# Performance work log

Measured on AMD Instinct MI355X. Metric: run time of the kernel, lower is better.

The kernel has to match this reference:

```python
import jax, jax.numpy as jnp
import numpy as np

# ---- geometry / physics constants (from setup_params) ----
H = 400; W_CROP = 400
PSF_W = 121          # interpolated_psf_width
CLEAR = 20           # clear_dist
_m = int(np.ceil(PSF_W / 2 - CLEAR + 2))
MARGIN = _m + _m % 2                    # 44
IM = H + 2 * MARGIN                     # 488
MAG = 100.0; PX_CCD = 11.0              # M, pixel_size_CCD
NZ = 64; Z_MIN = -2.0; Z_MAX = 2.0      # psf bank z sampling
SIGMA_READ = 10.0                       # read noise std (counts)
N_EMIT = 2048


def setup_inputs() -> dict:
    key = jax.random.key(0)
    k1, k2, k3, k4 = jax.random.split(key, 4)
    # emitter positions (um): xy in [-15,15] (stays inside canvas), z in [-2,2]
    lo = jnp.array([-15.0, -15.0, Z_MIN], jnp.float32)
    hi = jnp.array([15.0, 15.0, Z_MAX], jnp.float32)
    local_xyz = jax.random.uniform(k1, (1, N_EMIT, 3), jnp.float32) * (hi - lo) + lo
    Nphotons = jax.random.uniform(k2, (1, N_EMIT), jnp.float32) * 4000.0 + 1000.0
    xy_center = jnp.zeros((2,), jnp.float32)  # FOV center; unused when fd_flag=False
    psf_bank = jax.random.uniform(k3, (NZ, PSF_W, PSF_W), jnp.float32)  # positive PSFs
    noise_map = jax.random.normal(k4, (H, W_CROP), jnp.float32)         # unit gaussians
    return {"local_xyz": local_xyz, "Nphotons": Nphotons, "xy_center": xy_center,
            "psf_bank": psf_bank, "noise_map": noise_map}


def reference(local_xyz, Nphotons, xy_center, psf_bank, noise_map):
    x = local_xyz[0, :, 0]                       # [N] um
    y = local_xyz[0, :, 1]
    z = local_xyz[0, :, 2]
    nph = Nphotons[0]                            # [N]

    # psf_module(0,0,z): nearest-z lookup in precomputed bank (fd_flag=False)
    zi = jnp.clip(jnp.round((z - Z_MIN) / (Z_MAX - Z_MIN) * (NZ - 1)),
                  0, NZ - 1).astype(jnp.int32)
    psf = psf_bank[zi]                           # [N, PSF_W, PSF_W]

    # emitter position in camera pixels
    lx = x * MAG / PX_CCD
    ly = y * MAG / PX_CCD
    r0f = ly + IM / 2 - PSF_W / 2
    c0f = lx + IM / 2 - PSF_W / 2
    r0 = jnp.floor(r0f).astype(jnp.int32)        # [N] integer splat origin
    c0 = jnp.floor(c0f).astype(jnp.int32)
    rs = (r0f - jnp.floor(r0f))[:, None, None]   # sub-pixel shift in [0,1)
    cs = (c0f - jnp.floor(c0f))[:, None, None]

    # sub-pixel shift (bilinear, zero-fill boundary): out[i,j] = in[i-rs, j-cs]
    P = jnp.pad(psf, ((0, 0), (1, 0), (1, 0)))
    sh = ((1 - rs) * (1 - cs) * P[:, 1:, 1:] + rs * (1 - cs) * P[:, :-1, 1:]
          + (1 - rs) * cs * P[:, 1:, :-1] + rs * cs * P[:, :-1, :-1])
    sh = jnp.abs(sh)
    sh = sh / sh.sum(axis=(1, 2), keepdims=True) * nph[:, None, None]

    # scatter-add splat into shared canvas
    ar = jnp.arange(PSF_W, dtype=jnp.int32)
    rows = r0[:, None, None] + ar[None, :, None]  # [N, PSF_W, 1]
    cols = c0[:, None, None] + ar[None, None, :]  # [N, 1, PSF_W]
    canvas = jnp.zeros((IM, IM), sh.dtype).at[rows, cols].add(sh)

    im = canvas[MARGIN:MARGIN + H, MARGIN:MARGIN + W_CROP]

    # NoiseLayer: Gaussian approx of Poisson shot + read noise
    im_noisy = im + jnp.sqrt(jnp.maximum(im, 0.0) + SIGMA_READ ** 2) * noise_map

    # project_01 normalization
    return (im_noisy - im_noisy.min()) / (im_noisy.max() - im_noisy.min())
```

## Files before the change

### kernel.cpp

```cpp
#include <hip/hip_runtime.h>

#define H        400
#define W_CROP   400
#define PSF_W    121
#define MARGIN   44
#define IM       488
#define NZ       64
#define N_EMIT   2048
#define PSF_AREA (PSF_W * PSF_W)
#define SIGMA2   100.0f
#define TILE     16
#define TB       25
#define NTILES   (TB * TB)
#define NPIX     (H * W_CROP)
#define PADW     152
#define PADA     (PADW * PADW)
#define CHUNKS   4
#define CAPC     224
#define CAP_B    512
#define NBUCK    (TB * CHUNKS)
#define PADBLK   512

static __device__ __forceinline__ unsigned enc_ord(float f) {
    unsigned u = __float_as_uint(f);
    return (u & 0x80000000u) ? ~u : (u | 0x80000000u);
}
static __device__ __forceinline__ float dec_ord(unsigned u) {
    return __uint_as_float((u & 0x80000000u) ? (u & 0x7fffffffu) : ~u);
}

static __device__ __forceinline__ void geom_of(const float* __restrict__ xyz, int e,
                                               int& r0, int& c0, int& zi,
                                               float& r0f, float& c0f) {
    const float x = xyz[3 * e + 0];
    const float y = xyz[3 * e + 1];
    const float z = xyz[3 * e + 2];
    const float lx = (x * 100.0f) / 11.0f;
    const float ly = (y * 100.0f) / 11.0f;
    r0f = (ly + 244.0f) - 60.5f;
    c0f = (lx + 244.0f) - 60.5f;
    r0 = (int)floorf(r0f);
    c0 = (int)floorf(c0f);
    zi = (int)rintf((z + 2.0f) / 4.0f * 63.0f);
    zi = min(max(zi, 0), NZ - 1);
}

__global__ __launch_bounds__(256) void prep_kernel(
        const float* __restrict__ psf_bank, float* __restrict__ zpart,
        float* __restrict__ pad, unsigned* __restrict__ minmax,
        const float* __restrict__ xyz, const float* __restrict__ nph_arr,
        float4* __restrict__ bucket, int* __restrict__ bcnt)
{
    __shared__ float red[4][4];
    __shared__ int   wtot[4];

    if (blockIdx.x < PADBLK) {
        const int zi   = blockIdx.x >> 3;
        const int part = blockIdx.x & 7;

        if (blockIdx.x == 0 && threadIdx.x == 0) { minmax[0] = 0xFFFFFFFFu; minmax[1] = 0u; }

        const float* __restrict__ src = psf_bank + (size_t)zi * PSF_AREA;
        float* __restrict__ dst = pad + (size_t)zi * PADA;

        const int plo = part * 2888;
        const int phi = min(plo + 2888, PADA);
        for (int i = plo + (int)threadIdx.x; i < phi; i += 256) {
            const int rp = i / PADW;
            const int r = rp - 16;
            const int c = i - rp * PADW - 16;
            const bool in = ((unsigned)r < (unsigned)PSF_W) && ((unsigned)c < (unsigned)PSF_W);
            dst[i] = in ? src[r * PSF_W + c] : 0.0f;
        }

        const int slo = part * 1831;
        const int shi = min(slo + 1831, PSF_AREA);
        float S = 0.f, R = 0.f, C = 0.f, K = 0.f;
        for (int i = slo + (int)threadIdx.x; i < shi; i += 256) {
            const float v = src[i];
            const int r = i / PSF_W;
            const int c = i - r * PSF_W;
            S += v;
            if (r == PSF_W - 1) R += v;
            if (c == PSF_W - 1) C += v;
            if (r == PSF_W - 1 && c == PSF_W - 1) K += v;
        }
        #pragma unroll
        for (int off = 32; off > 0; off >>= 1) {
            S += __shfl_down(S, off, 64);
            R += __shfl_down(R, off, 64);
            C += __shfl_down(C, off, 64);
            K += __shfl_down(K, off, 64);
        }
        const int wave = threadIdx.x >> 6, lane = threadIdx.x & 63;
        if (lane == 0) { red[wave][0] = S; red[wave][1] = R; red[wave][2] = C; red[wave][3] = K; }
        __syncthreads();
        if (threadIdx.x == 0) {
            float4 o;
            o.x = (red[0][0] + red[1][0]) + (red[2][0] + red[3][0]);
            o.y = (red[0][1] + red[1][1]) + (red[2][1] + red[3][1]);
            o.z = (red[0][2] + red[1][2]) + (red[2][2] + red[3][2]);
            o.w = (red[0][3] + red[1][3]) + (red[2][3] + red[3][3]);
            *(float4*)(zpart + (size_t)(zi * 8 + part) * 4) = o;
        }
        return;
    }

    const int b   = blockIdx.x - PADBLK;
    const int btr = b >> 2, bzc = b & 3;
    const int w    = threadIdx.x >> 6;
    const int lane = threadIdx.x & 63;

    int mycnt = 0;
    unsigned mymask = 0u;
    #pragma unroll
    for (int q = 0; q < 8; ++q) {
        const int e = (int)threadIdx.x * 8 + q;
        int r0, c0, zi; float r0f, c0f;
        geom_of(xyz, e, r0, c0, zi, r0f, c0f);
        const bool p = ((zi >> 4) == bzc)
                     && (btr >= ((r0 - MARGIN) >> 4)) && (btr <= ((r0 + 76) >> 4));
        mymask |= (unsigned)p << q;
        mycnt += (int)p;
    }

    int incl = mycnt;
    #pragma unroll
    for (int off = 1; off < 64; off <<= 1) {
        const int v = __shfl_up(incl, off, 64);
        if (lane >= off) incl += v;
    }
    if (lane == 63) wtot[w] = incl;
    __syncthreads();
    int base = incl - mycnt;
    #pragma unroll
    for (int ww = 0; ww < 4; ++ww) base += (ww < w) ? wtot[ww] : 0;
    const int ntot = wtot[0] + wtot[1] + wtot[2] + wtot[3];

    if (mymask) {
        int slot = base;
        #pragma unroll
        for (int q = 0; q < 8; ++q) {
            if (mymask & (1u << q)) {
                const int e = (int)threadIdx.x * 8 + q;
                int r0, c0, zi; float r0f, c0f;
                geom_of(xyz, e, r0, c0, zi, r0f, c0f);
                if (slot < CAP_B) {
                    const float rs = r0f - floorf(r0f);
                    const float cs = c0f - floorf(c0f);
                    const float nph = nph_arr[e];
                    float4 s0, s1;
                    s0.x = nph * (1.0f - rs) * (1.0f - cs);
                    s0.y = nph * (1.0f - rs) * cs;
                    s0.z = nph * rs * (1.0f - cs);
                    s0.w = nph * rs * cs;
                    const int packed = ((r0 + 16) << 15) | ((c0 + 16) << 6) | zi;
                    s1.x = rs; s1.y = cs; s1.z = __int_as_float(packed); s1.w = 0.f;
                    bucket[(size_t)(b * CAP_B + slot) * 2]     = s0;
                    bucket[(size_t)(b * CAP_B + slot) * 2 + 1] = s1;
                }
                ++slot;
            }
        }
    }
    if (threadIdx.x == 0) bcnt[b] = min(ntot, CAP_B);
}

__global__ __launch_bounds__(256) void gather_kernel(
        const float* __restrict__ pad, const float4* __restrict__ bucket,
        const int* __restrict__ bcnt, const float* __restrict__ zpart,
        float* __restrict__ parts)
{
    const int zc   = (blockIdx.x & 7) >> 1;
    const int tile = 2 * (blockIdx.x >> 3) + (blockIdx.x & 1);
    if (tile >= NTILES) return;

    __shared__ float4 smeta[2 * CAPC];
    __shared__ float  tilepart[4][256];
    __shared__ int    wtot[4];

    const int tr = tile / TB, tc = tile - tr * TB;
    const int w    = threadIdx.x >> 6;
    const int lane = threadIdx.x & 63;
    const int px = lane & 15;
    const int wy = lane >> 4;
    const int orow0 = tr * TILE + wy * 4;
    const int ocol  = tc * TILE + px;
    const int crow0 = orow0 + MARGIN;
    const int ccol  = ocol + MARGIN;
    const int tcb   = (crow0 * PADW + ccol) * 4;
    const char* __restrict__ pbase = (const char*)pad;

    const int b   = tr * CHUNKS + zc;
    const int n_b = bcnt[b];
    const float4* __restrict__ bk = bucket + (size_t)b * CAP_B * 2;

    int nstaged = 0;
    for (int base_i = 0; base_i < n_b; base_i += 256) {
        const int i = base_i + (int)threadIdx.x;
        float4 m0, m1;
        int r0 = 0, c0 = 0, zi = 0;
        bool p = false;
        if (i < n_b) {
            m0 = bk[2 * i];
            m1 = bk[2 * i + 1];
            const int packed = __float_as_int(m1.z);
            zi = packed & 63;
            c0 = ((packed >> 6) & 511) - 16;
            r0 = ((packed >> 15) & 511) - 16;
            p = (tc >= ((c0 - MARGIN) >> 4)) && (tc <= ((c0 + 76) >> 4));
        }
        int incl = (int)p;
        #pragma unroll
        for (int off = 1; off < 64; off <<= 1) {
            const int v = __shfl_up(incl, off, 64);
            if (lane >= off) incl += v;
        }
        if (lane == 63) wtot[w] = incl;
        __syncthreads();
        int slot = nstaged + incl - (int)p;
        #pragma unroll
        for (int ww = 0; ww < 4; ++ww) slot += (ww < w) ? wtot[ww] : 0;
        const int round_tot = wtot[0] + wtot[1] + wtot[2] + wtot[3];
        if (p && slot < CAPC) {
            const float rs = m1.x, cs = m1.y;
            const float4* __restrict__ zp = (const float4*)zpart + zi * 8;
            float4 zm = zp[0];
            #pragma unroll
            for (int u = 1; u < 8; ++u) {
                const float4 t = zp[u];
                zm.x += t.x; zm.y += t.y; zm.z += t.z; zm.w += t.w;
            }
            const float ssum = zm.x - rs * zm.y - cs * zm.z + rs * cs * zm.w;
            const float inv = 1.0f / ssum;
            float4 s0, s1;
            s0.x = m0.x * inv; s0.y = m0.y * inv; s0.z = m0.z * inv; s0.w = m0.w * inv;
            const int offb = (zi * PADA + (15 - r0) * PADW + (16 - c0)) * 4;
            s1.x = __int_as_float(offb);
            s1.y = __int_as_float(r0);
            s1.z = __int_as_float(c0);
            s1.w = 0.f;
            smeta[2 * slot]     = s0;
            smeta[2 * slot + 1] = s1;
        }
        nstaged += round_tot;
        __syncthreads();
    }
    const int n = min(nstaged, CAPC);

    float acc0[4] = {0.f, 0.f, 0.f, 0.f};
    float acc1[4] = {0.f, 0.f, 0.f, 0.f};
    float acc2[4] = {0.f, 0.f, 0.f, 0.f};
    float acc3[4] = {0.f, 0.f, 0.f, 0.f};

    auto body = [&](int j, float* acc) {
        const float4 wt = smeta[2 * j];
        const float4 mm = smeta[2 * j + 1];
        const int off = __float_as_int(mm.x);
        const int pr0 = crow0 - __float_as_int(mm.y);
        const int pc  = ccol  - __float_as_int(mm.z);
        const char* __restrict__ p = pbase + (tcb + off);
        float a[5], b2[5];
        #pragma unroll
        for (int i = 0; i < 5; ++i) a[i] = *(const float*)(p + i * (PADW * 4));
        #pragma unroll
        for (int i = 0; i < 5; ++i) b2[i] = __shfl_up(a[i], 1, 16);
        if (px == 0) {
            #pragma unroll
            for (int i = 0; i < 5; ++i) b2[i] = *(const float*)(p - 4 + i * (PADW * 4));
        }
        const bool pcok = (unsigned)pc <= 120u;
        #pragma unroll
        for (int k = 0; k < 4; ++k) {
            float v = wt.x * a[k + 1];
            v = fmaf(wt.y, b2[k + 1], v);
            v = fmaf(wt.z, a[k],      v);
            v = fmaf(wt.w, b2[k],     v);
            const bool ok = pcok & ((unsigned)(pr0 + k) <= 120u);
            acc[k] += ok ? v : 0.f;
        }
    };

    int j = w;
    for (; j + 12 < n; j += 16) {
        body(j, acc0); body(j + 4, acc1); body(j + 8, acc2); body(j + 12, acc3);
    }
    for (; j < n; j += 4) body(j, acc0);

    #pragma unroll
    for (int k = 0; k < 4; ++k)
        tilepart[w][(wy * 4 + k) * 16 + px] = (acc0[k] + acc1[k]) + (acc2[k] + acc3[k]);
    __syncthreads();

    const int row = threadIdx.x >> 4, col = threadIdx.x & 15;
    const float s = ((tilepart[0][threadIdx.x] + tilepart[1][threadIdx.x]) +
                     (tilepart[2][threadIdx.x] + tilepart[3][threadIdx.x]));
    parts[(size_t)zc * NPIX + (tr * TILE + row) * W_CROP + (tc * TILE + col)] = s;
}

__global__ __launch_bounds__(256) void noise_minmax_kernel(
        const float* __restrict__ parts, const float* __restrict__ noise,
        float* __restrict__ out, unsigned* __restrict__ minmax)
{
    const int i = blockIdx.x * 256 + threadIdx.x;
    float vmin = 1e30f, vmax = -1e30f;
    if (i < NPIX / 4) {
        const float4 p0 = ((const float4*)parts)[i];
        const float4 p1 = ((const float4*)(parts + NPIX))[i];
        const float4 p2 = ((const float4*)(parts + 2 * NPIX))[i];
        const float4 p3 = ((const float4*)(parts + 3 * NPIX))[i];
        float4 im;
        im.x = (p0.x + p1.x) + (p2.x + p3.x);
        im.y = (p0.y + p1.y) + (p2.y + p3.y);
        im.z = (p0.z + p1.z) + (p2.z + p3.z);
        im.w = (p0.w + p1.w) + (p2.w + p3.w);
        const float4 nz = ((const float4*)noise)[i];
        im.x += sqrtf(fmaxf(im.x, 0.f) + SIGMA2) * nz.x;
        im.y += sqrtf(fmaxf(im.y, 0.f) + SIGMA2) * nz.y;
        im.z += sqrtf(fmaxf(im.z, 0.f) + SIGMA2) * nz.z;
        im.w += sqrtf(fmaxf(im.w, 0.f) + SIGMA2) * nz.w;
        ((float4*)out)[i] = im;
        vmin = fminf(fminf(im.x, im.y), fminf(im.z, im.w));
        vmax = fmaxf(fmaxf(im.x, im.y), fmaxf(im.z, im.w));
    }
    #pragma unroll
    for (int off = 32; off > 0; off >>= 1) {
        vmin = fminf(vmin, __shfl_down(vmin, off, 64));
        vmax = fmaxf(vmax, __shfl_down(vmax, off, 64));
    }
    if ((threadIdx.x & 63) == 0) {
        atomicMin(&minmax[0], enc_ord(vmin));
        atomicMax(&minmax[1], enc_ord(vmax));
    }
}

__global__ __launch_bounds__(256) void finalize_kernel(float* __restrict__ out,
                                                       const unsigned* __restrict__ minmax)
{
    const int i = blockIdx.x * 256 + threadIdx.x;
    if (i >= NPIX / 4) return;
    const float mn = dec_ord(minmax[0]);
    const float inv = 1.0f / (dec_ord(minmax[1]) - mn);
    float4 v = ((float4*)out)[i];
    v.x = (v.x - mn) * inv;
    v.y = (v.y - mn) * inv;
    v.z = (v.z - mn) * inv;
    v.w = (v.w - mn) * inv;
    ((float4*)out)[i] = v;
}

extern "C" void kernel_launch(void* const* d_in, const int* in_sizes, int n_in,
                              void* d_out, int out_size, void* d_ws, size_t ws_size,
                              hipStream_t stream) {
    const float* xyz      = (const float*)d_in[0];
    const float* nph      = (const float*)d_in[1];
    const float* psf_bank = (const float*)d_in[3];
    const float* noise    = (const float*)d_in[4];
    float* out = (float*)d_out;

    char* ws = (char*)d_ws;
    unsigned* minmax = (unsigned*)(ws + 0);
    float*    zpart  = (float*)(ws + 1024);
    float*    pad    = (float*)(ws + 9216);
    float4*   bucket = (float4*)(ws + 5923840);
    int*      bcnt   = (int*)(ws + 7562240);
    float*    parts  = (float*)(ws + 7563264);

    prep_kernel<<<PADBLK + NBUCK, 256, 0, stream>>>(psf_bank, zpart, pad, minmax,
                                                    xyz, nph, bucket, bcnt);
    gather_kernel<<<2504, 256, 0, stream>>>(pad, bucket, bcnt, zpart, parts);
    noise_minmax_kernel<<<(NPIX / 4 + 255) / 256, 256, 0, stream>>>(parts, noise, out, minmax);
    finalize_kernel<<<(NPIX / 4 + 255) / 256, 256, 0, stream>>>(out, minmax);
}
```

Baseline: 65.03 us.

## Split prep into pad and bucket kernels, precompute normalized weights in bucket stage

```diff
diff --git a/kernel.cpp b/kernel.cpp
--- a/kernel.cpp
+++ b/kernel.cpp
@@ -19,7 +19,6 @@
 #define CAPC     224
 #define CAP_B    512
 #define NBUCK    (TB * CHUNKS)
-#define PADBLK   512
 
 static __device__ __forceinline__ unsigned enc_ord(float f) {
     unsigned u = __float_as_uint(f);
@@ -45,68 +44,61 @@
     zi = min(max(zi, 0), NZ - 1);
 }
 
-__global__ __launch_bounds__(256) void prep_kernel(
+__global__ __launch_bounds__(256) void pad_zsum_kernel(
         const float* __restrict__ psf_bank, float* __restrict__ zpart,
-        float* __restrict__ pad, unsigned* __restrict__ minmax,
+        float* __restrict__ pad, unsigned* __restrict__ minmax)
+{
+    __shared__ float red[4][4];
+    const int zi   = blockIdx.x >> 3;
+    const int part = blockIdx.x & 7;
+
+    if (blockIdx.x == 0 && threadIdx.x == 0) { minmax[0] = 0xFFFFFFFFu; minmax[1] = 0u; }
+
+    const float* __restrict__ src = psf_bank + (size_t)zi * PSF_AREA;
+    float* __restrict__ dst = pad + (size_t)zi * PADA;
+
+    const int plo = part * 2888;
+    const int phi = min(plo + 2888, PADA);
+    float S = 0.f, R = 0.f, C = 0.f, K = 0.f;
+    for (int i = plo + (int)threadIdx.x; i < phi; i += 256) {
+        const int rp = i / PADW;
+        const int r = rp - 16;
+        const int c = i - rp * PADW - 16;
+        const bool in = ((unsigned)r < (unsigned)PSF_W) && ((unsigned)c < (unsigned)PSF_W);
+        const float v = in ? src[r * PSF_W + c] : 0.0f;
+        dst[i] = v;
+        S += v;
+        if (r == PSF_W - 1) R += v;
+        if (c == PSF_W - 1) C += v;
+        if (r == PSF_W - 1 && c == PSF_W - 1) K += v;
+    }
+    #pragma unroll
+    for (int off = 32; off > 0; off >>= 1) {
+        S += __shfl_down(S, off, 64);
+        R += __shfl_down(R, off, 64);
+        C += __shfl_down(C, off, 64);
+        K += __shfl_down(K, off, 64);
+    }
+    const int wave = threadIdx.x >> 6, lane = threadIdx.x & 63;
+    if (lane == 0) { red[wave][0] = S; red[wave][1] = R; red[wave][2] = C; red[wave][3] = K; }
+    __syncthreads();
+    if (threadIdx.x == 0) {
+        float4 o;
+        o.x = (red[0][0] + red[1][0]) + (red[2][0] + red[3][0]);
+        o.y = (red[0][1] + red[1][1]) + (red[2][1] + red[3][1]);
+        o.z = (red[0][2] + red[1][2]) + (red[2][2] + red[3][2]);
+        o.w = (red[0][3] + red[1][3]) + (red[2][3] + red[3][3]);
+        *(float4*)(zpart + (size_t)(zi * 8 + part) * 4) = o;
+    }
+}
+
+__global__ __launch_bounds__(256) void bucket_kernel(
         const float* __restrict__ xyz, const float* __restrict__ nph_arr,
+        const float* __restrict__ zpart,
         float4* __restrict__ bucket, int* __restrict__ bcnt)
 {
-    __shared__ float red[4][4];
-    __shared__ int   wtot[4];
-
-    if (blockIdx.x < PADBLK) {
-        const int zi   = blockIdx.x >> 3;
-        const int part = blockIdx.x & 7;
-
-        if (blockIdx.x == 0 && threadIdx.x == 0) { minmax[0] = 0xFFFFFFFFu; minmax[1] = 0u; }
-
-        const float* __restrict__ src = psf_bank + (size_t)zi * PSF_AREA;
-        float* __restrict__ dst = pad + (size_t)zi * PADA;
-
-        const int plo = part * 2888;
-        const int phi = min(plo + 2888, PADA);
-        for (int i = plo + (int)threadIdx.x; i < phi; i += 256) {
-            const int rp = i / PADW;
-            const int r = rp - 16;
-            const int c = i - rp * PADW - 16;
-            const bool in = ((unsigned)r < (unsigned)PSF_W) && ((unsigned)c < (unsigned)PSF_W);
-            dst[i] = in ? src[r * PSF_W + c] : 0.0f;
-        }
-
-        const int slo = part * 1831;
-        const int shi = min(slo + 1831, PSF_AREA);
-        float S = 0.f, R = 0.f, C = 0.f, K = 0.f;
-        for (int i = slo + (int)threadIdx.x; i < shi; i += 256) {
-            const float v = src[i];
-            const int r = i / PSF_W;
-            const int c = i - r * PSF_W;
-            S += v;
-            if (r == PSF_W - 1) R += v;
-            if (c == PSF_W - 1) C += v;
-            if (r == PSF_W - 1 && c == PSF_W - 1) K += v;
-        }
-        #pragma unroll
-        for (int off = 32; off > 0; off >>= 1) {
-            S += __shfl_down(S, off, 64);
-            R += __shfl_down(R, off, 64);
-            C += __shfl_down(C, off, 64);
-            K += __shfl_down(K, off, 64);
-        }
-        const int wave = threadIdx.x >> 6, lane = threadIdx.x & 63;
-        if (lane == 0) { red[wave][0] = S; red[wave][1] = R; red[wave][2] = C; red[wave][3] = K; }
-        __syncthreads();
-        if (threadIdx.x == 0) {
-            float4 o;
-            o.x = (red[0][0] + red[1][0]) + (red[2][0] + red[3][0]);
-            o.y = (red[0][1] + red[1][1]) + (red[2][1] + red[3][1]);
-            o.z = (red[0][2] + red[1][2]) + (red[2][2] + red[3][2]);
-            o.w = (red[0][3] + red[1][3]) + (red[2][3] + red[3][3]);
-            *(float4*)(zpart + (size_t)(zi * 8 + part) * 4) = o;
-        }
-        return;
-    }
-
-    const int b   = blockIdx.x - PADBLK;
+    __shared__ int wtot[4];
+    const int b   = blockIdx.x;
     const int btr = b >> 2, bzc = b & 3;
     const int w    = threadIdx.x >> 6;
     const int lane = threadIdx.x & 63;
@@ -148,14 +140,25 @@
                 if (slot < CAP_B) {
                     const float rs = r0f - floorf(r0f);
                     const float cs = c0f - floorf(c0f);
-                    const float nph = nph_arr[e];
+                    const float4* __restrict__ zp = (const float4*)zpart + zi * 8;
+                    float4 zm = zp[0];
+                    #pragma unroll
+                    for (int u = 1; u < 8; ++u) {
+                        const float4 t = zp[u];
+                        zm.x += t.x; zm.y += t.y; zm.z += t.z; zm.w += t.w;
+                    }
+                    const float ssum = zm.x - rs * zm.y - cs * zm.z + rs * cs * zm.w;
+                    const float s = nph_arr[e] / ssum;
                     float4 s0, s1;
-                    s0.x = nph * (1.0f - rs) * (1.0f - cs);
-                    s0.y = nph * (1.0f - rs) * cs;
-                    s0.z = nph * rs * (1.0f - cs);
-                    s0.w = nph * rs * cs;
-                    const int packed = ((r0 + 16) << 15) | ((c0 + 16) << 6) | zi;
-                    s1.x = rs; s1.y = cs; s1.z = __int_as_float(packed); s1.w = 0.f;
+                    s0.x = s * (1.0f - rs) * (1.0f - cs);
+                    s0.y = s * (1.0f - rs) * cs;
+                    s0.z = s * rs * (1.0f - cs);
+                    s0.w = s * rs * cs;
+                    const int offb = (zi * PADA + (15 - r0) * PADW + (16 - c0)) * 4;
+                    s1.x = __int_as_float(offb);
+                    s1.y = __int_as_float(r0);
+                    s1.z = __int_as_float(c0);
+                    s1.w = 0.f;
                     bucket[(size_t)(b * CAP_B + slot) * 2]     = s0;
                     bucket[(size_t)(b * CAP_B + slot) * 2 + 1] = s1;
                 }
@@ -168,8 +171,7 @@
 
 __global__ __launch_bounds__(256) void gather_kernel(
         const float* __restrict__ pad, const float4* __restrict__ bucket,
-        const int* __restrict__ bcnt, const float* __restrict__ zpart,
-        float* __restrict__ parts)
+        const int* __restrict__ bcnt, float* __restrict__ parts)
 {
     const int zc   = (blockIdx.x & 7) >> 1;
     const int tile = 2 * (blockIdx.x >> 3) + (blockIdx.x & 1);
@@ -199,49 +201,24 @@
     for (int base_i = 0; base_i < n_b; base_i += 256) {
         const int i = base_i + (int)threadIdx.x;
         float4 m0, m1;
-        int r0 = 0, c0 = 0, zi = 0;
         bool p = false;
         if (i < n_b) {
             m0 = bk[2 * i];
             m1 = bk[2 * i + 1];
-            const int packed = __float_as_int(m1.z);
-            zi = packed & 63;
-            c0 = ((packed >> 6) & 511) - 16;
-            r0 = ((packed >> 15) & 511) - 16;
+            const int c0 = __float_as_int(m1.z);
             p = (tc >= ((c0 - MARGIN) >> 4)) && (tc <= ((c0 + 76) >> 4));
         }
-        int incl = (int)p;
-        #pragma unroll
-        for (int off = 1; off < 64; off <<= 1) {
-            const int v = __shfl_up(incl, off, 64);
-            if (lane >= off) incl += v;
-        }
-        if (lane == 63) wtot[w] = incl;
+        const unsigned long long m = __ballot(p);
+        const int before = __popcll(m & ((1ULL << lane) - 1ULL));
+        if (lane == 63) wtot[w] = before + (int)p;
         __syncthreads();
-        int slot = nstaged + incl - (int)p;
+        int slot = nstaged + before;
         #pragma unroll
         for (int ww = 0; ww < 4; ++ww) slot += (ww < w) ? wtot[ww] : 0;
         const int round_tot = wtot[0] + wtot[1] + wtot[2] + wtot[3];
         if (p && slot < CAPC) {
-            const float rs = m1.x, cs = m1.y;
-            const float4* __restrict__ zp = (const float4*)zpart + zi * 8;
-            float4 zm = zp[0];
-            #pragma unroll
-            for (int u = 1; u < 8; ++u) {
-                const float4 t = zp[u];
-                zm.x += t.x; zm.y += t.y; zm.z += t.z; zm.w += t.w;
-            }
-            const float ssum = zm.x - rs * zm.y - cs * zm.z + rs * cs * zm.w;
-            const float inv = 1.0f / ssum;
-            float4 s0, s1;
-            s0.x = m0.x * inv; s0.y = m0.y * inv; s0.z = m0.z * inv; s0.w = m0.w * inv;
-            const int offb = (zi * PADA + (15 - r0) * PADW + (16 - c0)) * 4;
-            s1.x = __int_as_float(offb);
-            s1.y = __int_as_float(r0);
-            s1.z = __int_as_float(c0);
-            s1.w = 0.f;
-            smeta[2 * slot]     = s0;
-            smeta[2 * slot + 1] = s1;
+            smeta[2 * slot]     = m0;
+            smeta[2 * slot + 1] = m1;
         }
         nstaged += round_tot;
         __syncthreads();
@@ -366,9 +343,9 @@
     int*      bcnt   = (int*)(ws + 7562240);
     float*    parts  = (float*)(ws + 7563264);
 
-    prep_kernel<<<PADBLK + NBUCK, 256, 0, stream>>>(psf_bank, zpart, pad, minmax,
-                                                    xyz, nph, bucket, bcnt);
-    gather_kernel<<<2504, 256, 0, stream>>>(pad, bucket, bcnt, zpart, parts);
+    pad_zsum_kernel<<<NZ * 8, 256, 0, stream>>>(psf_bank, zpart, pad, minmax);
+    bucket_kernel<<<NBUCK, 256, 0, stream>>>(xyz, nph, zpart, bucket, bcnt);
+    gather_kernel<<<2504, 256, 0, stream>>>(pad, bucket, bcnt, parts);
     noise_minmax_kernel<<<(NPIX / 4 + 255) / 256, 256, 0, stream>>>(parts, noise, out, minmax);
     finalize_kernel<<<(NPIX / 4 + 255) / 256, 256, 0, stream>>>(out, minmax);
 }
```

Measured after the change: 70.09 us. 1.08x slower.
